# Optimization experiments

Hardware: AMD Instinct MI355X
Metric: run time of the kernel (lower is better)

The kernel has to match this reference:

```python
import jax, jax.numpy as jnp
import numpy as np

PH = PW = 16  # patch size


def setup_inputs() -> dict:
    key = jax.random.key(0)
    k1, k2, k3, k4, k5 = jax.random.split(key, 5)
    B, N, D, V = 8, 4096, 768, 10240
    x = jax.random.uniform(k1, (B, N, D), dtype=jnp.float32)          # (B, N, ph*pw*C) in [0,1)
    patch_coord = jax.random.randint(k2, (B, N, 2), 0, 64).astype(jnp.int64)  # (y, x) grid coords
    patch_valid = jax.random.randint(k3, (B, N), 0, 2).astype(bool)
    proj_w = jax.random.normal(k4, (D, D), dtype=jnp.float32) * 0.02  # Linear weight (out, in), no bias
    pos_table = jax.random.normal(k5, (2, V, D), dtype=jnp.float32) * 0.02
    return {"x": x, "patch_coord": patch_coord, "patch_valid": patch_valid,
            "proj_w": proj_w, "pos_table": pos_table}


def reference(x, patch_coord, patch_valid, proj_w, pos_table):
    B, N, PPC = x.shape
    C = PPC // (PH * PW)
    # Reorder patch pixels from (ph, pw, C) flat order to (C, ph, pw) flat order.
    x = x.reshape(B, N, PH, PW, C).transpose(0, 1, 4, 2, 3).reshape(B, N, PPC)
    x = 2.0 * (x - 0.5)
    x = jnp.einsum('bnk,dk->bnd', x, proj_w)  # Linear, bias=False
    # External (y, x) -> internal (x, y)
    position_ids = patch_coord[..., ::-1]
    clamped = jnp.maximum(position_ids, 0)
    # Equivalent to one_hot(clamped) @ table summed over the 2 coord axes.
    pos = pos_table[0][clamped[..., 0]] + pos_table[1][clamped[..., 1]]  # (B, N, D)
    padding_positions = ~patch_valid
    pos = jnp.where(padding_positions[..., None], 0.0, pos)
    return x + pos, position_ids, padding_positions
```

## Files before the change

### kernel.cpp

```cpp
#include <hip/hip_runtime.h>
#include <hip/hip_bf16.h>
#include <cstddef>

#define D_DIM 768
#define V_DIM 10240
#define ROWS 32768
#define BM 128
#define BN 128
#define BK 32

using bf16x8 = __attribute__((ext_vector_type(8))) __bf16;
using f32x4  = __attribute__((ext_vector_type(4))) float;

__global__ void prep_w(const float* __restrict__ W, __bf16* __restrict__ Wp,
                       float* __restrict__ bias) {
    int d = blockIdx.x;
    int t = threadIdx.x;
    float s = 0.f;
    for (int j = t; j < D_DIM; j += 256) {
        int c  = j % 3;
        int pw = (j / 3) & 15;
        int ph = j / 48;
        int k  = c * 256 + ph * 16 + pw;
        float w = W[d * D_DIM + k];
        Wp[d * D_DIM + j] = (__bf16)(2.0f * w);
        s += w;
    }
    __shared__ float red[256];
    red[t] = s;
    __syncthreads();
    for (int off = 128; off > 0; off >>= 1) {
        if (t < off) red[t] += red[t + off];
        __syncthreads();
    }
    if (t == 0) bias[d] = -red[0];
}

__global__ void aux_out(const int* __restrict__ coord, const int* __restrict__ valid,
                        float* __restrict__ out1, float* __restrict__ out2) {
    int i = blockIdx.x * blockDim.x + threadIdx.x;
    if (i < ROWS) {
        int c0 = coord[2 * i];
        int c1 = coord[2 * i + 1];
        out1[2 * i]     = (float)c1;
        out1[2 * i + 1] = (float)c0;
        out2[i] = valid[i] ? 0.0f : 1.0f;
    }
}

__launch_bounds__(256)
__global__ void gemm_pos(const float* __restrict__ X, const __bf16* __restrict__ Wp,
                         const float* __restrict__ bias, const float* __restrict__ ptab,
                         const int* __restrict__ coord, const int* __restrict__ valid,
                         float* __restrict__ out) {
    __shared__ __align__(16) __bf16 la[BM * BK];
    __shared__ __align__(16) __bf16 lb[BN * BK];

    const int n0 = blockIdx.x * BN;
    const int m0 = blockIdx.y * BM;

    const int tid  = threadIdx.x;
    const int lane = tid & 63;
    const int wave = tid >> 6;
    const int wr   = (wave >> 1) * 64;
    const int wc   = (wave & 1) * 64;
    const int lr   = lane & 15;
    const int kq   = (lane >> 4) * 8;

    f32x4 acc[4][4] = {};

    for (int kt = 0; kt < D_DIM / BK; ++kt) {
        const int k0 = kt * BK;

        #pragma unroll
        for (int i = 0; i < 2; ++i) {
            int idx = i * 2048 + tid * 8;
            int row = idx >> 5;
            int col = idx & 31;
            const __bf16* src = Wp + (size_t)(n0 + row) * D_DIM + k0 + col;
            __builtin_amdgcn_global_load_lds(
                (const __attribute__((address_space(1))) void*)src,
                (__attribute__((address_space(3))) void*)&lb[idx], 16, 0, 0);
        }

        #pragma unroll
        for (int i = 0; i < 2; ++i) {
            int idx = i * 2048 + tid * 8;
            int row = idx >> 5;
            int col = idx & 31;
            const float4* src = (const float4*)(X + (size_t)(m0 + row) * D_DIM + k0 + col);
            float4 f0 = src[0];
            float4 f1 = src[1];
            bf16x8 v;
            v[0] = (__bf16)f0.x; v[1] = (__bf16)f0.y; v[2] = (__bf16)f0.z; v[3] = (__bf16)f0.w;
            v[4] = (__bf16)f1.x; v[5] = (__bf16)f1.y; v[6] = (__bf16)f1.z; v[7] = (__bf16)f1.w;
            *(bf16x8*)&la[idx] = v;
        }

        __syncthreads();

        bf16x8 af[4], bfr[4];
        #pragma unroll
        for (int i = 0; i < 4; ++i)
            af[i] = *(const bf16x8*)&la[(wr + i * 16 + lr) * BK + kq];
        #pragma unroll
        for (int j = 0; j < 4; ++j)
            bfr[j] = *(const bf16x8*)&lb[(wc + j * 16 + lr) * BK + kq];

        #pragma unroll
        for (int i = 0; i < 4; ++i)
            #pragma unroll
            for (int j = 0; j < 4; ++j)
                acc[i][j] = __builtin_amdgcn_mfma_f32_16x16x32_bf16(af[i], bfr[j], acc[i][j], 0, 0, 0);

        __syncthreads();
    }

    const float* pt0 = ptab;
    const float* pt1 = ptab + (size_t)V_DIM * D_DIM;
    const int rq = (lane >> 4) * 4;

    float bvals[4];
    #pragma unroll
    for (int j = 0; j < 4; ++j)
        bvals[j] = bias[n0 + wc + j * 16 + lr];

    #pragma unroll
    for (int i = 0; i < 4; ++i) {
        #pragma unroll
        for (int r = 0; r < 4; ++r) {
            int m = m0 + wr + i * 16 + rq + r;
            int c0 = coord[2 * m];
            int c1 = coord[2 * m + 1];
            if (c0 < 0) c0 = 0;
            if (c1 < 0) c1 = 0;
            int vld = valid[m];
            #pragma unroll
            for (int j = 0; j < 4; ++j) {
                int d = n0 + wc + j * 16 + lr;
                float v = acc[i][j][r] + bvals[j];
                if (vld)
                    v += pt0[(size_t)c1 * D_DIM + d] + pt1[(size_t)c0 * D_DIM + d];
                out[(size_t)m * D_DIM + d] = v;
            }
        }
    }
}

extern "C" void kernel_launch(void* const* d_in, const int* in_sizes, int n_in,
                              void* d_out, int out_size, void* d_ws, size_t ws_size,
                              hipStream_t stream) {
    const float* x     = (const float*)d_in[0];
    const int*   coord = (const int*)d_in[1];
    const int*   valid = (const int*)d_in[2];
    const float* W     = (const float*)d_in[3];
    const float* ptab  = (const float*)d_in[4];

    float* out0 = (float*)d_out;
    float* out1 = out0 + (size_t)ROWS * D_DIM;
    float* out2 = out1 + (size_t)ROWS * 2;

    __bf16* Wp  = (__bf16*)d_ws;
    float*  bias = (float*)((char*)d_ws + (size_t)D_DIM * D_DIM * sizeof(__bf16));

    hipLaunchKernelGGL(prep_w, dim3(D_DIM), dim3(256), 0, stream, W, Wp, bias);
    hipLaunchKernelGGL(aux_out, dim3(ROWS / 256), dim3(256), 0, stream, coord, valid, out1, out2);
    hipLaunchKernelGGL(gemm_pos, dim3(D_DIM / BN, ROWS / BM), dim3(256), 0, stream,
                       x, Wp, bias, ptab, coord, valid, out0);
}
```

Before: 304.2 us.

## Pre-convert X to bf16 in a separate pass and load A tiles via direct-to-LDS

Adds a pre-pass kernel that converts the fp32 input X to bf16 in workspace and also writes the auxiliary outputs. The GEMM then loads both A and B tiles with global_load_lds directly into shared memory, so the main loop no longer does fp32 loads, conversions and register-to-LDS stores. The aim is less per-tile instruction overhead and less register pressure in the GEMM. The cost is an extra full read of X plus a write and re-read of a 48MB bf16 copy. The old path is kept as a fallback when the workspace is too small.

Result: faster. 286.4 us (-5.9%).

```diff
diff --git a/kernel.cpp b/kernel.cpp
--- a/kernel.cpp
+++ b/kernel.cpp
@@ -36,6 +36,28 @@
     if (t == 0) bias[d] = -red[0];
 }
 
+__global__ void conv_aux(const float* __restrict__ X, __bf16* __restrict__ Xb,
+                         const int* __restrict__ coord, const int* __restrict__ valid,
+                         float* __restrict__ out1, float* __restrict__ out2) {
+    int i = blockIdx.x * blockDim.x + threadIdx.x;
+    size_t base = (size_t)i * 8;
+    const float4* src = (const float4*)(X + base);
+    float4 f0 = src[0];
+    float4 f1 = src[1];
+    bf16x8 v;
+    v[0] = (__bf16)f0.x; v[1] = (__bf16)f0.y; v[2] = (__bf16)f0.z; v[3] = (__bf16)f0.w;
+    v[4] = (__bf16)f1.x; v[5] = (__bf16)f1.y; v[6] = (__bf16)f1.z; v[7] = (__bf16)f1.w;
+    *(bf16x8*)(Xb + base) = v;
+
+    if (i < ROWS) {
+        int c0 = coord[2 * i];
+        int c1 = coord[2 * i + 1];
+        out1[2 * i]     = (float)c1;
+        out1[2 * i + 1] = (float)c0;
+        out2[i] = valid[i] ? 0.0f : 1.0f;
+    }
+}
+
 __global__ void aux_out(const int* __restrict__ coord, const int* __restrict__ valid,
                         float* __restrict__ out1, float* __restrict__ out2) {
     int i = blockIdx.x * blockDim.x + threadIdx.x;
@@ -49,10 +71,99 @@
 }
 
 __launch_bounds__(256)
-__global__ void gemm_pos(const float* __restrict__ X, const __bf16* __restrict__ Wp,
-                         const float* __restrict__ bias, const float* __restrict__ ptab,
-                         const int* __restrict__ coord, const int* __restrict__ valid,
-                         float* __restrict__ out) {
+__global__ void gemm_fast(const __bf16* __restrict__ Xb, const __bf16* __restrict__ Wp,
+                          const float* __restrict__ bias, const float* __restrict__ ptab,
+                          const int* __restrict__ coord, const int* __restrict__ valid,
+                          float* __restrict__ out) {
+    __shared__ __align__(16) __bf16 la[BM * BK];
+    __shared__ __align__(16) __bf16 lb[BN * BK];
+
+    const int n0 = blockIdx.x * BN;
+    const int m0 = blockIdx.y * BM;
+
+    const int tid  = threadIdx.x;
+    const int lane = tid & 63;
+    const int wave = tid >> 6;
+    const int wr   = (wave >> 1) * 64;
+    const int wc   = (wave & 1) * 64;
+    const int lr   = lane & 15;
+    const int kq   = (lane >> 4) * 8;
+
+    f32x4 acc[4][4] = {};
+
+    for (int kt = 0; kt < D_DIM / BK; ++kt) {
+        const int k0 = kt * BK;
+
+        #pragma unroll
+        for (int i = 0; i < 2; ++i) {
+            int idx = i * 2048 + tid * 8;
+            int row = idx >> 5;
+            int col = idx & 31;
+            const __bf16* srcA = Xb + (size_t)(m0 + row) * D_DIM + k0 + col;
+            __builtin_amdgcn_global_load_lds(
+                (const __attribute__((address_space(1))) void*)srcA,
+                (__attribute__((address_space(3))) void*)&la[idx], 16, 0, 0);
+            const __bf16* srcB = Wp + (size_t)(n0 + row) * D_DIM + k0 + col;
+            __builtin_amdgcn_global_load_lds(
+                (const __attribute__((address_space(1))) void*)srcB,
+                (__attribute__((address_space(3))) void*)&lb[idx], 16, 0, 0);
+        }
+
+        __syncthreads();
+
+        bf16x8 af[4], bfr[4];
+        #pragma unroll
+        for (int i = 0; i < 4; ++i)
+            af[i] = *(const bf16x8*)&la[(wr + i * 16 + lr) * BK + kq];
+        #pragma unroll
+        for (int j = 0; j < 4; ++j)
+            bfr[j] = *(const bf16x8*)&lb[(wc + j * 16 + lr) * BK + kq];
+
+        #pragma unroll
+        for (int i = 0; i < 4; ++i)
+            #pragma unroll
+            for (int j = 0; j < 4; ++j)
+                acc[i][j] = __builtin_amdgcn_mfma_f32_16x16x32_bf16(af[i], bfr[j], acc[i][j], 0, 0, 0);
+
+        __syncthreads();
+    }
+
+    const float* pt0 = ptab;
+    const float* pt1 = ptab + (size_t)V_DIM * D_DIM;
+    const int rq = (lane >> 4) * 4;
+
+    float bvals[4];
+    #pragma unroll
+    for (int j = 0; j < 4; ++j)
+        bvals[j] = bias[n0 + wc + j * 16 + lr];
+
+    #pragma unroll
+    for (int i = 0; i < 4; ++i) {
+        #pragma unroll
+        for (int r = 0; r < 4; ++r) {
+            int m = m0 + wr + i * 16 + rq + r;
+            int c0 = coord[2 * m];
+            int c1 = coord[2 * m + 1];
+            if (c0 < 0) c0 = 0;
+            if (c1 < 0) c1 = 0;
+            int vld = valid[m];
+            #pragma unroll
+            for (int j = 0; j < 4; ++j) {
+                int d = n0 + wc + j * 16 + lr;
+                float v = acc[i][j][r] + bvals[j];
+                if (vld)
+                    v += pt0[(size_t)c1 * D_DIM + d] + pt1[(size_t)c0 * D_DIM + d];
+                out[(size_t)m * D_DIM + d] = v;
+            }
+        }
+    }
+}
+
+__launch_bounds__(256)
+__global__ void gemm_slow(const float* __restrict__ X, const __bf16* __restrict__ Wp,
+                          const float* __restrict__ bias, const float* __restrict__ ptab,
+                          const int* __restrict__ coord, const int* __restrict__ valid,
+                          float* __restrict__ out) {
     __shared__ __align__(16) __bf16 la[BM * BK];
     __shared__ __align__(16) __bf16 lb[BN * BK];
 
@@ -160,11 +271,27 @@
     float* out1 = out0 + (size_t)ROWS * D_DIM;
     float* out2 = out1 + (size_t)ROWS * 2;
 
-    __bf16* Wp  = (__bf16*)d_ws;
-    float*  bias = (float*)((char*)d_ws + (size_t)D_DIM * D_DIM * sizeof(__bf16));
-
-    hipLaunchKernelGGL(prep_w, dim3(D_DIM), dim3(256), 0, stream, W, Wp, bias);
-    hipLaunchKernelGGL(aux_out, dim3(ROWS / 256), dim3(256), 0, stream, coord, valid, out1, out2);
-    hipLaunchKernelGGL(gemm_pos, dim3(D_DIM / BN, ROWS / BM), dim3(256), 0, stream,
-                       x, Wp, bias, ptab, coord, valid, out0);
-}
+    const size_t xb_bytes = (size_t)ROWS * D_DIM * sizeof(__bf16);
+    const size_t wp_bytes = (size_t)D_DIM * D_DIM * sizeof(__bf16);
+    const size_t need = xb_bytes + wp_bytes + D_DIM * sizeof(float);
+
+    if (ws_size >= need) {
+        __bf16* Xb  = (__bf16*)d_ws;
+        __bf16* Wp  = (__bf16*)((char*)d_ws + xb_bytes);
+        float* bias = (float*)((char*)d_ws + xb_bytes + wp_bytes);
+
+        hipLaunchKernelGGL(prep_w, dim3(D_DIM), dim3(256), 0, stream, W, Wp, bias);
+        hipLaunchKernelGGL(conv_aux, dim3((ROWS * D_DIM / 8) / 256), dim3(256), 0, stream,
+                           x, Xb, coord, valid, out1, out2);
+        hipLaunchKernelGGL(gemm_fast, dim3(D_DIM / BN, ROWS / BM), dim3(256), 0, stream,
+                           Xb, Wp, bias, ptab, coord, valid, out0);
+    } else {
+        __bf16* Wp  = (__bf16*)d_ws;
+        float* bias = (float*)((char*)d_ws + wp_bytes);
+
+        hipLaunchKernelGGL(prep_w, dim3(D_DIM), dim3(256), 0, stream, W, Wp, bias);
+        hipLaunchKernelGGL(aux_out, dim3(ROWS / 256), dim3(256), 0, stream, coord, valid, out1, out2);
+        hipLaunchKernelGGL(gemm_slow, dim3(D_DIM / BN, ROWS / BM), dim3(256), 0, stream,
+                           x, Wp, bias, ptab, coord, valid, out0);
+    }
+}
```
